# Kernel optimization log

Measured on AMD Instinct MI355X. Metric: run time of the kernel, lower is better.

The kernel has to match this reference:

```python
import jax, jax.numpy as jnp
import numpy as np

B, T, E, H = 2, 2048, 1024, 16


def setup_inputs() -> dict:
    key = jax.random.key(0)
    ks = jax.random.split(key, 8)
    # VarianceScaling(1.0) ~ truncated normal with stddev ~ sqrt(1/fan_in)
    std = 1.0 / np.sqrt(E)
    x = jax.random.normal(ks[0], (B, T, E), dtype=jnp.float32)
    y = jax.random.normal(ks[1], (B, T, E), dtype=jnp.float32)
    # causal mask [1, 1, T, T]
    mask = jnp.tril(jnp.ones((T, T), dtype=jnp.float32))[None, None]
    Wq = jax.random.normal(ks[2], (E, E), dtype=jnp.float32) * std
    Wk = jax.random.normal(ks[3], (E, E), dtype=jnp.float32) * std
    Wv = jax.random.normal(ks[4], (E, E), dtype=jnp.float32) * std
    Wo = jax.random.normal(ks[5], (E, E), dtype=jnp.float32) * std
    bq = jnp.zeros((E,), jnp.float32)
    bk = jnp.zeros((E,), jnp.float32)
    bv = jnp.zeros((E,), jnp.float32)
    bo = jnp.zeros((E,), jnp.float32)
    return {"x": x, "y": y, "mask": mask, "Wq": Wq, "bq": bq,
            "Wk": Wk, "bk": bk, "Wv": Wv, "bv": bv, "Wo": Wo, "bo": bo,
            "num_heads": H}


def reference(x, y, mask, Wq, bq, Wk, bk, Wv, bv, Wo, bo, num_heads):
    Bx, Tq, Emb = x.shape
    Tkv = y.shape[1]
    d = Emb // num_heads
    q = (x @ Wq + bq).reshape(Bx, Tq, num_heads, d)
    k = (y @ Wk + bk).reshape(Bx, Tkv, num_heads, d)
    v = (y @ Wv + bv).reshape(Bx, Tkv, num_heads, d)
    scale = 1.0 / np.sqrt(d).astype(np.float32)
    att = scale * jnp.einsum('bthd,bThd->bhtT', q, k)  # [B,H,Tq,Tkv]
    att = att * mask - 1e10 * (1.0 - mask)
    att = jax.nn.softmax(att, axis=-1)
    out = jnp.einsum('bhtT,bThd->bthd', att, v).reshape(Bx, Tq, Emb)
    return out @ Wo + bo
```

## Files before the change

kernel.cpp:

```cpp
#include <hip/hip_runtime.h>
#include <stdint.h>

#define BB 2
#define TT 2048
#define EE 1024
#define HH 16
#define DD 64
#define MM (BB*TT)

typedef unsigned short u16;
typedef __attribute__((ext_vector_type(4))) float f32x4;
typedef __attribute__((ext_vector_type(8))) __bf16 bf16x8;
typedef __attribute__((ext_vector_type(8))) u16 u16x8;
typedef __attribute__((ext_vector_type(4))) u16 u16x4;

union FragU { u16x8 u; bf16x8 b; };
union BfU { __bf16 h; u16 u; };

__device__ __forceinline__ u16 f2bf(float f) {
  uint32_t u = __float_as_uint(f);
  u += 0x7fffu + ((u >> 16) & 1u);
  return (u16)(u >> 16);
}

__global__ __launch_bounds__(256) void prep(const float* __restrict__ x, const float* __restrict__ y,
                                            const float* __restrict__ Wq, const float* __restrict__ Wk,
                                            const float* __restrict__ Wv, const float* __restrict__ Wo,
                                            u16* __restrict__ xb, u16* __restrict__ yb,
                                            u16* __restrict__ Wqt, u16* __restrict__ Wkvt,
                                            u16* __restrict__ Wot) {
  __shared__ alignas(16) float tile[64][65];
  int bi = blockIdx.x, t = threadIdx.x;
  if (bi < 4096) {
    const float* src = (bi < 2048) ? x : y;
    u16* dst = (bi < 2048) ? xb : yb;
    int i = (bi & 2047) * 256 + t;
    const f32x4* s4 = (const f32x4*)src;
    f32x4 a = s4[2*i], b = s4[2*i+1];
    u16x8 o;
    o[0]=f2bf(a[0]); o[1]=f2bf(a[1]); o[2]=f2bf(a[2]); o[3]=f2bf(a[3]);
    o[4]=f2bf(b[0]); o[5]=f2bf(b[1]); o[6]=f2bf(b[2]); o[7]=f2bf(b[3]);
    ((u16x8*)dst)[i] = o;
    return;
  }
  int wi = bi - 4096;
  int z = wi >> 8;
  const float* W; u16* Tp;
  switch (z) {
    case 0: W = Wq; Tp = Wqt; break;
    case 1: W = Wk; Tp = Wkvt; break;
    case 2: W = Wv; Tp = Wkvt + (size_t)1024*EE; break;
    default: W = Wo; Tp = Wot; break;
  }
  int r8 = wi & 255;
  int n0 = (r8 & 15) * 64, k0 = (r8 >> 4) * 64;
#pragma unroll
  for (int i = 0; i < 16; ++i) {
    int idx = i*256 + t; int r = idx >> 6, c = idx & 63;
    tile[r][c] = W[(size_t)(k0 + r) * EE + n0 + c];
  }
  __syncthreads();
#pragma unroll
  for (int i = 0; i < 16; ++i) {
    int idx = i*256 + t; int rn = idx >> 6, ck = idx & 63;
    Tp[(size_t)(n0 + rn) * EE + k0 + ck] = f2bf(tile[ck][rn]);
  }
}

template <int EPI>
__device__ __forceinline__ void gemm_body(const u16* __restrict__ A, const u16* __restrict__ Bt,
                                          const float* __restrict__ bias, void* __restrict__ Cout,
                                          int N, int K, float oscale, int bm, int bn,
                                          u16 (*As)[72], u16 (*Bs)[72]) {
  const int t = threadIdx.x;
  const int lane = t & 63, wave = t >> 6;
  const int wr = wave >> 1, wc = wave & 1;

  f32x4 acc[2][4] = {};

  const int srow = t >> 3;
  const int scol = (t & 7) * 8;
  const u16* Ag = A + (size_t)(bm * 64) * K;
  const u16* Bg = Bt + (size_t)(bn * 128) * K;

  u16x8 ra[2], rb[4];
#pragma unroll
  for (int r = 0; r < 2; ++r)
    ra[r] = *(const u16x8*)(Ag + (size_t)(r*32 + srow) * K + scol);
#pragma unroll
  for (int r = 0; r < 4; ++r)
    rb[r] = *(const u16x8*)(Bg + (size_t)(r*32 + srow) * K + scol);

  const int nk = K / 64;
  for (int kt = 0; kt < nk; ++kt) {
    __syncthreads();
#pragma unroll
    for (int r = 0; r < 2; ++r) *(u16x8*)&As[r*32 + srow][scol] = ra[r];
#pragma unroll
    for (int r = 0; r < 4; ++r) *(u16x8*)&Bs[r*32 + srow][scol] = rb[r];
    __syncthreads();
    if (kt + 1 < nk) {
      const int k0 = (kt + 1) * 64;
#pragma unroll
      for (int r = 0; r < 2; ++r)
        ra[r] = *(const u16x8*)(Ag + (size_t)(r*32 + srow) * K + k0 + scol);
#pragma unroll
      for (int r = 0; r < 4; ++r)
        rb[r] = *(const u16x8*)(Bg + (size_t)(r*32 + srow) * K + k0 + scol);
    }
#pragma unroll
    for (int ks = 0; ks < 2; ++ks) {
      const int kc = ks*32 + ((lane >> 4) << 3);
      FragU af[2], bfr[4];
#pragma unroll
      for (int mi = 0; mi < 2; ++mi)
        af[mi].u = *(const u16x8*)&As[wr*32 + mi*16 + (lane & 15)][kc];
#pragma unroll
      for (int nj = 0; nj < 4; ++nj)
        bfr[nj].u = *(const u16x8*)&Bs[wc*64 + nj*16 + (lane & 15)][kc];
#pragma unroll
      for (int mi = 0; mi < 2; ++mi)
#pragma unroll
        for (int nj = 0; nj < 4; ++nj)
          acc[mi][nj] = __builtin_amdgcn_mfma_f32_16x16x32_bf16(af[mi].b, bfr[nj].b, acc[mi][nj], 0, 0, 0);
    }
  }

  const int cbase = bn*128 + wc*64 + (lane & 15);
  float bv[4];
#pragma unroll
  for (int nj = 0; nj < 4; ++nj) bv[nj] = bias[cbase + nj*16];
#pragma unroll
  for (int mi = 0; mi < 2; ++mi) {
    int row0 = bm*64 + wr*32 + mi*16 + ((lane >> 4) << 2);
    if (EPI == 2) {
      int bb = row0 >> 11;
      int tt = row0 & 2047;
      int tb64 = tt & ~63;
      int w6 = tt & 63;
      int p = ((w6 >> 5) << 5) | (((w6 >> 2) & 3) << 3) | (((w6 >> 4) & 1) << 2);
#pragma unroll
      for (int nj = 0; nj < 4; ++nj) {
        int cc = cbase + nj*16;
        int hh = cc >> 6, dd = cc & 63;
        u16x4 v;
#pragma unroll
        for (int i = 0; i < 4; ++i) v[i] = f2bf(acc[mi][nj][i] + bv[nj]);
        *(u16x4*)((u16*)Cout + ((size_t)((bb*HH + hh)*DD + dd))*2048 + tb64 + p) = v;
      }
    } else {
#pragma unroll
      for (int i = 0; i < 4; ++i) {
        if (EPI == 1) {
          float* Cp = (float*)Cout + (size_t)(row0 + i) * N + cbase;
#pragma unroll
          for (int nj = 0; nj < 4; ++nj)
            Cp[nj*16] = (acc[mi][nj][i] + bv[nj]) * oscale;
        } else {
          u16* Cp = (u16*)Cout + (size_t)(row0 + i) * N + cbase;
#pragma unroll
          for (int nj = 0; nj < 4; ++nj)
            Cp[nj*16] = f2bf((acc[mi][nj][i] + bv[nj]) * oscale);
        }
      }
    }
  }
}

__global__ __launch_bounds__(256) void gemm_qkv(const u16* __restrict__ xb, const u16* __restrict__ yb,
                                                const u16* __restrict__ Wqt, const u16* __restrict__ Wkvt,
                                                const float* __restrict__ bq, const float* __restrict__ bk,
                                                const float* __restrict__ bv,
                                                u16* __restrict__ Qb, u16* __restrict__ Kb,
                                                u16* __restrict__ Vtb, float c1) {
  __shared__ alignas(16) u16 As[64][72];
  __shared__ alignas(16) u16 Bs[128][72];
  const int i = blockIdx.x;
  const int l = (i & 7) * 192 + (i >> 3);
  const int bm = l / 24, bx = l % 24;
  if (bx < 8)
    gemm_body<0>(xb, Wqt, bq, Qb, 1024, EE, c1, bm, bx, As, Bs);
  else if (bx < 16)
    gemm_body<0>(yb, Wkvt, bk, Kb, 1024, EE, 1.0f, bm, bx - 8, As, Bs);
  else
    gemm_body<2>(yb, Wkvt + (size_t)1024*EE, bv, Vtb, 1024, EE, 1.0f, bm, bx - 16, As, Bs);
}

__global__ __launch_bounds__(256) void gemm_o(const u16* __restrict__ Atb, const u16* __restrict__ Wot,
                                              const float* __restrict__ bo, float* __restrict__ out) {
  __shared__ alignas(16) u16 As[64][72];
  __shared__ alignas(16) u16 Bs[128][72];
  const int i = blockIdx.x;
  const int l = (i & 7) * 64 + (i >> 3);
  const int bm = l / 8, bn = l % 8;
  gemm_body<1>(Atb, Wot, bo, out, 1024, EE, 1.0f, bm, bn, As, Bs);
}

__global__ __launch_bounds__(512, 4) void attn(const u16* __restrict__ Q, const u16* __restrict__ Kb,
                                               const u16* __restrict__ Vt, u16* __restrict__ O) {
  const int i0 = blockIdx.x;
  const int qq = i0 >> 8, a = (i0 >> 5) & 7, bh = i0 & 31;
  int qt;
  switch (qq) {
    case 0:  qt = 31 - a; break;
    case 1:  qt = 16 + a; break;
    case 2:  qt = 15 - a; break;
    default: qt = a;      break;
  }
  const int b = bh >> 4, h = bh & 15;

  const int t = threadIdx.x, lane = t & 63, w = t >> 6;
  const int ws_ = w & 3;
  const int hi = w >> 2;
  const int g = lane >> 4, c = lane & 15;
  __shared__ alignas(16) u16 Ks[2][64][72];
  __shared__ alignas(16) u16 Vs[2][64][72];

  const int qw0 = qt * 64 + ws_ * 16;

  FragU qf[2];
  const u16* Qbase = Q + ((size_t)(b*TT) + qw0) * EE + h*DD;
#pragma unroll
  for (int ks = 0; ks < 2; ++ks)
    qf[ks].u = *(const u16x8*)(Qbase + (size_t)c * EE + ks*32 + g*8);

  f32x4 oacc[4] = {};
  float l_part = 0.f;
  float m_run = -1e30f;

  const u16* Kbase = Kb + (size_t)(b*TT) * 1024 + h*DD;
  const u16* Vtbase = Vt + (size_t)(b*HH + h) * DD * 2048;

  const int nkv = qt + 1;
  const int npair = (nkv + 1) >> 1;

  const int srow = t >> 3;
  const int scol = (t & 7) * 8;

  u16x8 rk[2], rv[2];
  rk[0] = *(const u16x8*)(Kbase + (size_t)srow * 1024 + scol);
  rv[0] = *(const u16x8*)(Vtbase + (size_t)srow * 2048 + scol);
  if (1 < nkv) {
    rk[1] = *(const u16x8*)(Kbase + (size_t)(64 + srow) * 1024 + scol);
    rv[1] = *(const u16x8*)(Vtbase + (size_t)srow * 2048 + 64 + scol);
  }

  for (int jj = 0; jj < npair; ++jj) {
    const int j0 = 2*jj;
    __syncthreads();
    *(u16x8*)&Ks[0][srow][scol] = rk[0];
    *(u16x8*)&Vs[0][srow][scol] = rv[0];
    if (j0 + 1 < nkv) {
      *(u16x8*)&Ks[1][srow][scol] = rk[1];
      *(u16x8*)&Vs[1][srow][scol] = rv[1];
    }
    __syncthreads();
    if (jj + 1 < npair) {
      const int jn = 2*(jj + 1);
      rk[0] = *(const u16x8*)(Kbase + (size_t)(jn*64 + srow) * 1024 + scol);
      rv[0] = *(const u16x8*)(Vtbase + (size_t)srow * 2048 + jn*64 + scol);
      if (jn + 1 < nkv) {
        rk[1] = *(const u16x8*)(Kbase + (size_t)((jn+1)*64 + srow) * 1024 + scol);
        rv[1] = *(const u16x8*)(Vtbase + (size_t)srow * 2048 + (jn+1)*64 + scol);
      }
    }
    const int j = j0 + hi;
    const int kv0 = j * 64;
    if (j >= nkv || kv0 > qw0 + 15) continue;

    f32x4 s[4] = {};
    __builtin_amdgcn_s_setprio(1);
#pragma unroll
    for (int ks = 0; ks < 2; ++ks) {
      const int kc = ks*32 + g*8;
      FragU kf[4];
#pragma unroll
      for (int nj = 0; nj < 4; ++nj)
        kf[nj].u = *(const u16x8*)&Ks[hi][nj*16 + c][kc];
#pragma unroll
      for (int nj = 0; nj < 4; ++nj)
        s[nj] = __builtin_amdgcn_mfma_f32_16x16x32_bf16(kf[nj].b, qf[ks].b, s[nj], 0, 0, 0);
    }
    __builtin_amdgcn_s_setprio(0);

    const bool full = (kv0 + 63 <= qw0);
    float vmax;
    if (full) {
      float m0 = fmaxf(fmaxf(s[0][0], s[0][1]), fmaxf(s[0][2], s[0][3]));
      float m1 = fmaxf(fmaxf(s[1][0], s[1][1]), fmaxf(s[1][2], s[1][3]));
      float m2 = fmaxf(fmaxf(s[2][0], s[2][1]), fmaxf(s[2][2], s[2][3]));
      float m3 = fmaxf(fmaxf(s[3][0], s[3][1]), fmaxf(s[3][2], s[3][3]));
      vmax = fmaxf(fmaxf(m0, m1), fmaxf(m2, m3));
    } else {
      const int q = qw0 + c;
      vmax = -1e30f;
#pragma unroll
      for (int nj = 0; nj < 4; ++nj)
#pragma unroll
        for (int r = 0; r < 4; ++r) {
          float xv = s[nj][r];
          if (kv0 + nj*16 + 4*g + r > q) xv = -1e30f;
          s[nj][r] = xv;
          vmax = fmaxf(vmax, xv);
        }
    }

    if (__any(vmax > m_run + 8.f)) {
      float vm = vmax;
      vm = fmaxf(vm, __shfl_xor(vm, 1));
      vm = fmaxf(vm, __shfl_xor(vm, 2));
      vm = fmaxf(vm, __shfl_xor(vm, 4));
      vm = fmaxf(vm, __shfl_xor(vm, 8));
      vm = fmaxf(vm, __shfl_xor(vm, 16));
      vm = fmaxf(vm, __shfl_xor(vm, 32));
      float f = exp2f(m_run - vm);
      l_part *= f;
#pragma unroll
      for (int dj = 0; dj < 4; ++dj)
#pragma unroll
        for (int i = 0; i < 4; ++i) oacc[dj][i] *= f;
      m_run = vm;
    }

    FragU pa[2];
    float psum = 0.f;
#pragma unroll
    for (int nj = 0; nj < 4; ++nj)
#pragma unroll
      for (int r = 0; r < 4; ++r) {
        float p = exp2f(s[nj][r] - m_run);
        psum += p;
        BfU cv; cv.h = (__bf16)p;
        pa[nj >> 1].u[(nj & 1) * 4 + r] = cv.u;
      }
    l_part += psum;

    __builtin_amdgcn_s_setprio(1);
#pragma unroll
    for (int ks = 0; ks < 2; ++ks) {
#pragma unroll
      for (int dj = 0; dj < 4; ++dj) {
        FragU vf;
        vf.u = *(const u16x8*)&Vs[hi][dj*16 + c][ks*32 + g*8];
        oacc[dj] = __builtin_amdgcn_mfma_f32_16x16x32_bf16(pa[ks].b, vf.b, oacc[dj], 0, 0, 0);
      }
    }
    __builtin_amdgcn_s_setprio(0);
  }

  __syncthreads();
  l_part += __shfl_xor(l_part, 16);
  l_part += __shfl_xor(l_part, 32);

  float* mO = (float*)&Ks[0][0][0];
  float* mL = (float*)&Vs[0][0][0];

  if (hi) {
#pragma unroll
    for (int i = 0; i < 4; ++i) {
      int row = 4*g + i;
#pragma unroll
      for (int dj = 0; dj < 4; ++dj)
        mO[((size_t)(ws_*16 + row))*66 + dj*16 + c] = oacc[dj][i];
    }
    if (lane < 16) mL[ws_*16 + lane] = l_part;
    if (lane == 0) mL[64 + ws_] = m_run;
  }
  __syncthreads();
  if (!hi) {
    float m1 = mL[64 + ws_];
    float l1 = mL[ws_*16 + c];
    float mN = fmaxf(m_run, m1);
    float f0 = exp2f(m_run - mN);
    float f1 = exp2f(m1 - mN);
    float lm = l_part * f0 + l1 * f1;
    u16* Ob = O + ((size_t)(b*TT) + qw0) * EE + h*DD;
#pragma unroll
    for (int i = 0; i < 4; ++i) {
      int row = 4*g + i;
      float li = __shfl(lm, row);
      float inv = 1.f / li;
#pragma unroll
      for (int dj = 0; dj < 4; ++dj) {
        float o1 = mO[((size_t)(ws_*16 + row))*66 + dj*16 + c];
        Ob[(size_t)row * EE + dj*16 + c] = f2bf((oacc[dj][i] * f0 + o1 * f1) * inv);
      }
    }
  }
}

extern "C" void kernel_launch(void* const* d_in, const int* in_sizes, int n_in,
                              void* d_out, int out_size, void* d_ws, size_t ws_size,
                              hipStream_t stream) {
  const float* x  = (const float*)d_in[0];
  const float* y  = (const float*)d_in[1];
  const float* Wq = (const float*)d_in[3];
  const float* bq = (const float*)d_in[4];
  const float* Wk = (const float*)d_in[5];
  const float* bk = (const float*)d_in[6];
  const float* Wv = (const float*)d_in[7];
  const float* bv = (const float*)d_in[8];
  const float* Wo = (const float*)d_in[9];
  const float* bo = (const float*)d_in[10];

  if (ws_size < (size_t)58720256) return;

  char* ws = (char*)d_ws;
  u16* Wqt  = (u16*)(ws + 0);
  u16* Wkvt = (u16*)(ws + 2097152);
  u16* Wot  = (u16*)(ws + 6291456);
  u16* Qb   = (u16*)(ws + 8388608);
  u16* Kb   = (u16*)(ws + 16777216);
  u16* Vtb  = (u16*)(ws + 25165824);
  u16* Atb  = (u16*)(ws + 33554432);
  u16* xb   = (u16*)(ws + 41943040);
  u16* yb   = (u16*)(ws + 50331648);

  const float c1 = 0.125f * 1.44269504088896340736f;

  prep<<<5120, 256, 0, stream>>>(x, y, Wq, Wk, Wv, Wo, xb, yb, Wqt, Wkvt, Wot);
  gemm_qkv<<<1536, 256, 0, stream>>>(xb, yb, Wqt, Wkvt, bq, bk, bv, Qb, Kb, Vtb, c1);
  attn<<<1024, 512, 0, stream>>>(Qb, Kb, Vtb, Atb);
  gemm_o<<<512, 256, 0, stream>>>(Atb, Wot, bo, (float*)d_out);
}
```

Baseline: 117.1 us.

## Use direct global-to-LDS loads with XOR swizzle and larger QKV GEMM tiles

Replaces the register-staged global loads in the GEMM body with global_load_lds direct-to-LDS transfers, and swaps the padded LDS layout for an XOR-swizzled 64-wide one to avoid bank conflicts. The QKV projection GEMM now uses 128-row tiles, halving the grid to 768 blocks and raising reuse of the B tile. Register prefetch of the next k-tile is dropped, so loads are no longer overlapped with MFMA work within a block, relying on occupancy instead.

```diff
diff --git a/kernel.cpp b/kernel.cpp
--- a/kernel.cpp
+++ b/kernel.cpp
@@ -21,6 +21,11 @@
   uint32_t u = __float_as_uint(f);
   u += 0x7fffu + ((u >> 16) & 1u);
   return (u16)(u >> 16);
+}
+
+__device__ __forceinline__ void gload16(const u16* __restrict__ g, u16* l) {
+  __builtin_amdgcn_global_load_lds((const __attribute__((address_space(1))) void*)g,
+                                   (__attribute__((address_space(3))) void*)l, 16, 0, 0);
 }
 
 __global__ __launch_bounds__(256) void prep(const float* __restrict__ x, const float* __restrict__ y,
@@ -67,72 +72,68 @@
   }
 }
 
-template <int EPI>
+template <int BM, int EPI>
 __device__ __forceinline__ void gemm_body(const u16* __restrict__ A, const u16* __restrict__ Bt,
                                           const float* __restrict__ bias, void* __restrict__ Cout,
                                           int N, int K, float oscale, int bm, int bn,
-                                          u16 (*As)[72], u16 (*Bs)[72]) {
+                                          u16 (*As)[64], u16 (*Bs)[64]) {
+  constexpr int MI = BM / 32;
   const int t = threadIdx.x;
-  const int lane = t & 63, wave = t >> 6;
-  const int wr = wave >> 1, wc = wave & 1;
-
-  f32x4 acc[2][4] = {};
-
-  const int srow = t >> 3;
-  const int scol = (t & 7) * 8;
-  const u16* Ag = A + (size_t)(bm * 64) * K;
+  const int lane = t & 63, w = t >> 6;
+  const int wr = w >> 1, wc = w & 1;
+  const int g = lane >> 4, cl = lane & 15;
+
+  f32x4 acc[MI][4] = {};
+
+  const u16* Ag = A + (size_t)(bm * BM) * K;
   const u16* Bg = Bt + (size_t)(bn * 128) * K;
 
-  u16x8 ra[2], rb[4];
-#pragma unroll
-  for (int r = 0; r < 2; ++r)
-    ra[r] = *(const u16x8*)(Ag + (size_t)(r*32 + srow) * K + scol);
-#pragma unroll
-  for (int r = 0; r < 4; ++r)
-    rb[r] = *(const u16x8*)(Bg + (size_t)(r*32 + srow) * K + scol);
+  const int rl = lane >> 3;
+  const int sw = ((lane & 7) ^ rl) * 8;
 
   const int nk = K / 64;
   for (int kt = 0; kt < nk; ++kt) {
+    const int k0 = kt * 64;
     __syncthreads();
 #pragma unroll
-    for (int r = 0; r < 2; ++r) *(u16x8*)&As[r*32 + srow][scol] = ra[r];
-#pragma unroll
-    for (int r = 0; r < 4; ++r) *(u16x8*)&Bs[r*32 + srow][scol] = rb[r];
+    for (int j = 0; j < MI; ++j) {
+      int ca = w * MI + j;
+      gload16(Ag + (size_t)(ca*8 + rl) * K + k0 + sw, &As[ca*8][0]);
+    }
+#pragma unroll
+    for (int j = 0; j < 4; ++j) {
+      int cb = w * 4 + j;
+      gload16(Bg + (size_t)(cb*8 + rl) * K + k0 + sw, &Bs[cb*8][0]);
+    }
     __syncthreads();
-    if (kt + 1 < nk) {
-      const int k0 = (kt + 1) * 64;
-#pragma unroll
-      for (int r = 0; r < 2; ++r)
-        ra[r] = *(const u16x8*)(Ag + (size_t)(r*32 + srow) * K + k0 + scol);
-#pragma unroll
-      for (int r = 0; r < 4; ++r)
-        rb[r] = *(const u16x8*)(Bg + (size_t)(r*32 + srow) * K + k0 + scol);
-    }
 #pragma unroll
     for (int ks = 0; ks < 2; ++ks) {
-      const int kc = ks*32 + ((lane >> 4) << 3);
-      FragU af[2], bfr[4];
-#pragma unroll
-      for (int mi = 0; mi < 2; ++mi)
-        af[mi].u = *(const u16x8*)&As[wr*32 + mi*16 + (lane & 15)][kc];
-#pragma unroll
-      for (int nj = 0; nj < 4; ++nj)
-        bfr[nj].u = *(const u16x8*)&Bs[wc*64 + nj*16 + (lane & 15)][kc];
-#pragma unroll
-      for (int mi = 0; mi < 2; ++mi)
+      FragU af[MI], bfr[4];
+#pragma unroll
+      for (int mi = 0; mi < MI; ++mi) {
+        int row = wr*(BM/2) + mi*16 + cl;
+        af[mi].u = *(const u16x8*)&As[row][((ks*4 + g) ^ (row & 7)) * 8];
+      }
+#pragma unroll
+      for (int nj = 0; nj < 4; ++nj) {
+        int row = wc*64 + nj*16 + cl;
+        bfr[nj].u = *(const u16x8*)&Bs[row][((ks*4 + g) ^ (row & 7)) * 8];
+      }
+#pragma unroll
+      for (int mi = 0; mi < MI; ++mi)
 #pragma unroll
         for (int nj = 0; nj < 4; ++nj)
           acc[mi][nj] = __builtin_amdgcn_mfma_f32_16x16x32_bf16(af[mi].b, bfr[nj].b, acc[mi][nj], 0, 0, 0);
     }
   }
 
-  const int cbase = bn*128 + wc*64 + (lane & 15);
+  const int cbase = bn*128 + wc*64 + cl;
   float bv[4];
 #pragma unroll
   for (int nj = 0; nj < 4; ++nj) bv[nj] = bias[cbase + nj*16];
 #pragma unroll
-  for (int mi = 0; mi < 2; ++mi) {
-    int row0 = bm*64 + wr*32 + mi*16 + ((lane >> 4) << 2);
+  for (int mi = 0; mi < MI; ++mi) {
+    int row0 = bm*BM + wr*(BM/2) + mi*16 + (g << 2);
     if (EPI == 2) {
       int bb = row0 >> 11;
       int tt = row0 & 2047;
@@ -173,27 +174,27 @@
                                                 const float* __restrict__ bv,
                                                 u16* __restrict__ Qb, u16* __restrict__ Kb,
                                                 u16* __restrict__ Vtb, float c1) {
-  __shared__ alignas(16) u16 As[64][72];
-  __shared__ alignas(16) u16 Bs[128][72];
+  __shared__ alignas(16) u16 As[128][64];
+  __shared__ alignas(16) u16 Bs[128][64];
   const int i = blockIdx.x;
-  const int l = (i & 7) * 192 + (i >> 3);
+  const int l = (i & 7) * 96 + (i >> 3);
   const int bm = l / 24, bx = l % 24;
   if (bx < 8)
-    gemm_body<0>(xb, Wqt, bq, Qb, 1024, EE, c1, bm, bx, As, Bs);
+    gemm_body<128, 0>(xb, Wqt, bq, Qb, 1024, EE, c1, bm, bx, As, Bs);
   else if (bx < 16)
-    gemm_body<0>(yb, Wkvt, bk, Kb, 1024, EE, 1.0f, bm, bx - 8, As, Bs);
+    gemm_body<128, 0>(yb, Wkvt, bk, Kb, 1024, EE, 1.0f, bm, bx - 8, As, Bs);
   else
-    gemm_body<2>(yb, Wkvt + (size_t)1024*EE, bv, Vtb, 1024, EE, 1.0f, bm, bx - 16, As, Bs);
+    gemm_body<128, 2>(yb, Wkvt + (size_t)1024*EE, bv, Vtb, 1024, EE, 1.0f, bm, bx - 16, As, Bs);
 }
 
 __global__ __launch_bounds__(256) void gemm_o(const u16* __restrict__ Atb, const u16* __restrict__ Wot,
                                               const float* __restrict__ bo, float* __restrict__ out) {
-  __shared__ alignas(16) u16 As[64][72];
-  __shared__ alignas(16) u16 Bs[128][72];
+  __shared__ alignas(16) u16 As[64][64];
+  __shared__ alignas(16) u16 Bs[128][64];
   const int i = blockIdx.x;
   const int l = (i & 7) * 64 + (i >> 3);
   const int bm = l / 8, bn = l % 8;
-  gemm_body<1>(Atb, Wot, bo, out, 1024, EE, 1.0f, bm, bn, As, Bs);
+  gemm_body<64, 1>(Atb, Wot, bo, out, 1024, EE, 1.0f, bm, bn, As, Bs);
 }
 
 __global__ __launch_bounds__(512, 4) void attn(const u16* __restrict__ Q, const u16* __restrict__ Kb,
@@ -419,7 +420,7 @@
   const float c1 = 0.125f * 1.44269504088896340736f;
 
   prep<<<5120, 256, 0, stream>>>(x, y, Wq, Wk, Wv, Wo, xb, yb, Wqt, Wkvt, Wot);
-  gemm_qkv<<<1536, 256, 0, stream>>>(xb, yb, Wqt, Wkvt, bq, bk, bv, Qb, Kb, Vtb, c1);
+  gemm_qkv<<<768, 256, 0, stream>>>(xb, yb, Wqt, Wkvt, bq, bk, bv, Qb, Kb, Vtb, c1);
   attn<<<1024, 512, 0, stream>>>(Qb, Kb, Vtb, Atb);
   gemm_o<<<512, 256, 0, stream>>>(Atb, Wot, bo, (float*)d_out);
 }
```

Result: no change. 118.5 us (+1.2%).
